# Kernel optimization log

Hardware: AMD Instinct MI355X
Metric: run time of the kernel (lower is better)

The kernel has to match this reference:

```python
import jax, jax.numpy as jnp
import numpy as np

N_NODES = 100000
N_EDGES = 1600000
D_FEAT = 64


def setup_inputs() -> dict:
    key = jax.random.key(0)
    k1, k2, k3 = jax.random.split(key, 3)
    h = jax.random.normal(k1, (N_NODES, D_FEAT), dtype=jnp.float32)
    src = jax.random.randint(k2, (N_EDGES,), 0, N_NODES, dtype=jnp.int32)
    dst = jax.random.randint(k3, (N_EDGES,), 0, N_NODES, dtype=jnp.int32)
    edge_index = jnp.stack([src, dst], axis=0)  # [2, E]
    return {"h": h, "edge_index": edge_index}


def reference(h, edge_index):
    # EdgePassing: message = src node features (gather along edges)
    # Max_aggregation: per-dst-node max over incoming messages (segment max)
    src, dst = edge_index[0], edge_index[1]
    msgs = h[src]  # [E, D] gathered mailbox, never densified per-node
    agg = jax.ops.segment_max(msgs, dst, num_segments=N_NODES)  # [N, D]
    # DGL leaves nodes with no incoming messages at zero; segment_max yields -inf
    return jnp.where(jnp.isneginf(agg), jnp.zeros_like(agg), agg)
```

## Files before the change

### kernel.cpp

```cpp
#include <hip/hip_runtime.h>

#define D_FEAT 64
#define NEG_INF_BITS 0xFF800000u
#define ENC_NEG_INF  0x007FFFFFu
#define NPB 128
#define BSHIFT 7
#define TILE_E 4096
#define SP_BLOCK 512
#define BM_BLOCK 512
#define MAXB 1024

__device__ __forceinline__ unsigned enc_f32(float v) {
    unsigned b = __float_as_uint(v);
    return ((int)b >= 0) ? (b ^ 0x80000000u) : ~b;
}
__device__ __forceinline__ float dec_f32(unsigned u) {
    return (u & 0x80000000u) ? __uint_as_float(u ^ 0x80000000u) : __uint_as_float(~u);
}

__global__ void zero_kernel(int* __restrict__ p, int n) {
    int i = blockIdx.x * blockDim.x + threadIdx.x;
    if (i < n) p[i] = 0;
}

__global__ void hist_kernel(const int* __restrict__ dst, int* __restrict__ hist,
                            int E, int B) {
    __shared__ int lh[MAXB];
    for (int i = threadIdx.x; i < B; i += blockDim.x) lh[i] = 0;
    __syncthreads();
    int E4 = E >> 2;
    const int4* dst4 = (const int4*)dst;
    for (int i = blockIdx.x * blockDim.x + threadIdx.x; i < E4;
         i += gridDim.x * blockDim.x) {
        int4 d = dst4[i];
        atomicAdd(&lh[d.x >> BSHIFT], 1);
        atomicAdd(&lh[d.y >> BSHIFT], 1);
        atomicAdd(&lh[d.z >> BSHIFT], 1);
        atomicAdd(&lh[d.w >> BSHIFT], 1);
    }
    if (blockIdx.x == 0) {
        for (int i = (E4 << 2) + threadIdx.x; i < E; i += blockDim.x)
            atomicAdd(&lh[dst[i] >> BSHIFT], 1);
    }
    __syncthreads();
    for (int i = threadIdx.x; i < B; i += blockDim.x) {
        int c = lh[i];
        if (c) atomicAdd(&hist[i], c);
    }
}

__global__ void scan_kernel(const int* __restrict__ hist, int* __restrict__ bucket_start,
                            int* __restrict__ cursor, int B) {
    __shared__ int lds[MAXB];
    int tid = threadIdx.x;
    int v = (tid < B) ? hist[tid] : 0;
    lds[tid] = v;
    __syncthreads();
    for (int off = 1; off < MAXB; off <<= 1) {
        int t = (tid >= off) ? lds[tid - off] : 0;
        __syncthreads();
        lds[tid] += t;
        __syncthreads();
    }
    if (tid < B) {
        int excl = lds[tid] - v;
        bucket_start[tid] = excl;
        cursor[tid] = excl;
        if (tid == B - 1) bucket_start[B] = lds[tid];
    }
}

__global__ void scatter_pass_kernel(const int* __restrict__ src, const int* __restrict__ dst,
                                    int* __restrict__ cursor, unsigned* __restrict__ packed,
                                    int E, int B) {
    __shared__ int lcount[MAXB];
    __shared__ int lbase[MAXB];
    int tid = threadIdx.x;
    int base = blockIdx.x * TILE_E;
    int nE = min(TILE_E, E - base);

    for (int i = tid; i < B; i += SP_BLOCK) lcount[i] = 0;
    __syncthreads();

    int n4 = nE >> 2;
    const int4* dst4 = (const int4*)(dst + base);
    for (int k = tid; k < n4; k += SP_BLOCK) {
        int4 d = dst4[k];
        atomicAdd(&lcount[d.x >> BSHIFT], 1);
        atomicAdd(&lcount[d.y >> BSHIFT], 1);
        atomicAdd(&lcount[d.z >> BSHIFT], 1);
        atomicAdd(&lcount[d.w >> BSHIFT], 1);
    }
    for (int i = (n4 << 2) + tid; i < nE; i += SP_BLOCK)
        atomicAdd(&lcount[dst[base + i] >> BSHIFT], 1);
    __syncthreads();

    for (int b = tid; b < B; b += SP_BLOCK) {
        int c = lcount[b];
        lbase[b] = c ? atomicAdd(&cursor[b], c) : 0;
        lcount[b] = 0;
    }
    __syncthreads();

    for (int i = tid; i < nE; i += SP_BLOCK) {
        int d = dst[base + i];
        int b = d >> BSHIFT;
        int pos = lbase[b] + atomicAdd(&lcount[b], 1);
        packed[pos] = (unsigned)src[base + i] | ((unsigned)(d & (NPB - 1)) << 17);
    }
}

__global__ void __launch_bounds__(BM_BLOCK)
bucket_max_kernel(const float* __restrict__ h,
                  const int* __restrict__ bucket_start,
                  const unsigned* __restrict__ packed,
                  float* __restrict__ out, int N) {
    __shared__ unsigned buf[NPB * D_FEAT];
    int b = blockIdx.x;
    int tid = threadIdx.x;
    int node0 = b << BSHIFT;
    int nvals = (min(NPB, N - node0)) * D_FEAT;

    for (int i = tid; i < NPB * D_FEAT; i += BM_BLOCK) buf[i] = ENC_NEG_INF;
    __syncthreads();

    int beg = bucket_start[b];
    int end = bucket_start[b + 1];
    int wid = tid >> 6;
    int lane = tid & 63;

    for (int base = beg + (wid << 6); base < end; base += BM_BLOCK) {
        int nk = min(64, end - base);
        unsigned p = (lane < nk) ? packed[base + lane] : 0u;
        int j = 0;
        for (; j + 4 <= nk; j += 4) {
            unsigned p0 = (unsigned)__shfl((int)p, j);
            unsigned p1 = (unsigned)__shfl((int)p, j + 1);
            unsigned p2 = (unsigned)__shfl((int)p, j + 2);
            unsigned p3 = (unsigned)__shfl((int)p, j + 3);
            float v0 = h[(p0 & 0x1FFFFu) * D_FEAT + lane];
            float v1 = h[(p1 & 0x1FFFFu) * D_FEAT + lane];
            float v2 = h[(p2 & 0x1FFFFu) * D_FEAT + lane];
            float v3 = h[(p3 & 0x1FFFFu) * D_FEAT + lane];
            atomicMax(&buf[(p0 >> 17) * D_FEAT + lane], enc_f32(v0));
            atomicMax(&buf[(p1 >> 17) * D_FEAT + lane], enc_f32(v1));
            atomicMax(&buf[(p2 >> 17) * D_FEAT + lane], enc_f32(v2));
            atomicMax(&buf[(p3 >> 17) * D_FEAT + lane], enc_f32(v3));
        }
        for (; j < nk; ++j) {
            unsigned pj = (unsigned)__shfl((int)p, j);
            float v = h[(pj & 0x1FFFFu) * D_FEAT + lane];
            atomicMax(&buf[(pj >> 17) * D_FEAT + lane], enc_f32(v));
        }
    }
    __syncthreads();

    for (int i = tid; i < nvals; i += BM_BLOCK) {
        unsigned u = buf[i];
        out[node0 * D_FEAT + i] = (u == ENC_NEG_INF) ? 0.0f : dec_f32(u);
    }
}

__global__ void init_out_kernel(uint4* __restrict__ out, int n4) {
    int i = blockIdx.x * blockDim.x + threadIdx.x;
    if (i < n4) {
        uint4 v;
        v.x = NEG_INF_BITS; v.y = NEG_INF_BITS; v.z = NEG_INF_BITS; v.w = NEG_INF_BITS;
        out[i] = v;
    }
}
__global__ void scatter_max_kernel(const float* __restrict__ h, const int* __restrict__ src,
                                   const int* __restrict__ dst, float* __restrict__ out, int E) {
    int gid = blockIdx.x * blockDim.x + threadIdx.x;
    int e = gid >> 6;
    if (e >= E) return;
    int lane = gid & 63;
    float v = h[src[e] * D_FEAT + lane];
    int* addr = (int*)(out + dst[e] * D_FEAT + lane);
    if (v >= 0.0f) atomicMax(addr, __float_as_int(v));
    else           atomicMin((unsigned int*)addr, __float_as_uint(v));
}
__global__ void finalize_kernel(float* __restrict__ out, int n) {
    int i = blockIdx.x * blockDim.x + threadIdx.x;
    if (i < n && __float_as_uint(out[i]) == NEG_INF_BITS) out[i] = 0.0f;
}

extern "C" void kernel_launch(void* const* d_in, const int* in_sizes, int n_in,
                              void* d_out, int out_size, void* d_ws, size_t ws_size,
                              hipStream_t stream) {
    const float* h = (const float*)d_in[0];
    const int* edge_index = (const int*)d_in[1];
    int E = in_sizes[1] / 2;
    const int* src = edge_index;
    const int* dst = edge_index + E;
    float* out = (float*)d_out;
    int N = out_size / D_FEAT;

    int B = (N + NPB - 1) >> BSHIFT;
    size_t ws_needed = (size_t)(3 * B + 2 + E) * sizeof(int);

    if (N <= (1 << 17) && B <= MAXB && ws_size >= ws_needed) {
        int* hist         = (int*)d_ws;
        int* bucket_start = hist + B;
        int* cursor       = bucket_start + B + 1;
        unsigned* packed  = (unsigned*)(cursor + B);

        zero_kernel<<<(B + 255) / 256, 256, 0, stream>>>(hist, B);
        hist_kernel<<<512, 256, 0, stream>>>(dst, hist, E, B);
        scan_kernel<<<1, MAXB, 0, stream>>>(hist, bucket_start, cursor, B);
        int ntiles = (E + TILE_E - 1) / TILE_E;
        scatter_pass_kernel<<<ntiles, SP_BLOCK, 0, stream>>>(src, dst, cursor, packed, E, B);
        bucket_max_kernel<<<B, BM_BLOCK, 0, stream>>>(h, bucket_start, packed, out, N);
    } else {
        int n4 = out_size / 4;
        init_out_kernel<<<(n4 + 255) / 256, 256, 0, stream>>>((uint4*)out, n4);
        long long total = (long long)E * 64;
        scatter_max_kernel<<<(int)((total + 255) / 256), 256, 0, stream>>>(h, src, dst, out, E);
        finalize_kernel<<<(out_size + 255) / 256, 256, 0, stream>>>(out, out_size);
    }
}
```

Before: 178.1 us.

## Replace global-atomic bucket sort with per-tile counts and column scan

The bucketing pipeline now stores per-tile bucket counts in workspace, computes per-tile offsets with a column-wise wave scan, and places edges using those precomputed offsets. This removes the global zero kernel, the global histogram atomics and the per-tile global cursor atomics, and it avoids counting dst twice. Tiles become much larger (T=256 blocks), so placement has less parallelism and uses more workspace. The bucket_max gather loop is also unrolled from 4 to 8 so more loads are in flight.

After: 163.5 us. 1.09x faster.

```diff
diff --git a/kernel.cpp b/kernel.cpp
--- a/kernel.cpp
+++ b/kernel.cpp
@@ -5,8 +5,6 @@
 #define ENC_NEG_INF  0x007FFFFFu
 #define NPB 128
 #define BSHIFT 7
-#define TILE_E 4096
-#define SP_BLOCK 512
 #define BM_BLOCK 512
 #define MAXB 1024
 
@@ -18,39 +16,55 @@
     return (u & 0x80000000u) ? __uint_as_float(u ^ 0x80000000u) : __uint_as_float(~u);
 }
 
-__global__ void zero_kernel(int* __restrict__ p, int n) {
-    int i = blockIdx.x * blockDim.x + threadIdx.x;
-    if (i < n) p[i] = 0;
-}
-
-__global__ void hist_kernel(const int* __restrict__ dst, int* __restrict__ hist,
-                            int E, int B) {
+__global__ void count_kernel(const int* __restrict__ dst, int* __restrict__ counts,
+                             int E, int Te, int B) {
     __shared__ int lh[MAXB];
     for (int i = threadIdx.x; i < B; i += blockDim.x) lh[i] = 0;
     __syncthreads();
-    int E4 = E >> 2;
-    const int4* dst4 = (const int4*)dst;
-    for (int i = blockIdx.x * blockDim.x + threadIdx.x; i < E4;
-         i += gridDim.x * blockDim.x) {
-        int4 d = dst4[i];
+    int t = blockIdx.x;
+    int beg = t * Te;
+    int end = min(E, beg + Te);
+    int nE = (end > beg) ? (end - beg) : 0;
+    int n4 = nE >> 2;
+    const int4* d4 = (const int4*)(dst + beg);
+    for (int k = threadIdx.x; k < n4; k += blockDim.x) {
+        int4 d = d4[k];
         atomicAdd(&lh[d.x >> BSHIFT], 1);
         atomicAdd(&lh[d.y >> BSHIFT], 1);
         atomicAdd(&lh[d.z >> BSHIFT], 1);
         atomicAdd(&lh[d.w >> BSHIFT], 1);
     }
-    if (blockIdx.x == 0) {
-        for (int i = (E4 << 2) + threadIdx.x; i < E; i += blockDim.x)
-            atomicAdd(&lh[dst[i] >> BSHIFT], 1);
-    }
-    __syncthreads();
-    for (int i = threadIdx.x; i < B; i += blockDim.x) {
-        int c = lh[i];
-        if (c) atomicAdd(&hist[i], c);
-    }
+    for (int i = beg + (n4 << 2) + threadIdx.x; i < end; i += blockDim.x)
+        atomicAdd(&lh[dst[i] >> BSHIFT], 1);
+    __syncthreads();
+    for (int i = threadIdx.x; i < B; i += blockDim.x) counts[t * B + i] = lh[i];
+}
+
+__global__ void colscan_kernel(int* __restrict__ counts, int* __restrict__ hist,
+                               int T, int B) {
+    int w = (blockIdx.x * blockDim.x + threadIdx.x) >> 6;
+    int lane = threadIdx.x & 63;
+    if (w >= B) return;
+    int b = w;
+    int R = T >> 6;
+    int v[4], pre[4];
+    int base_t = lane * R;
+    for (int r = 0; r < R; ++r) v[r] = counts[(base_t + r) * B + b];
+    int s = 0;
+    for (int r = 0; r < R; ++r) { pre[r] = s; s += v[r]; }
+    int incl = s;
+    for (int off = 1; off < 64; off <<= 1) {
+        int tup = __shfl_up(incl, off);
+        if (lane >= off) incl += tup;
+    }
+    int excl = incl - s;
+    for (int r = 0; r < R; ++r) counts[(base_t + r) * B + b] = excl + pre[r];
+    int total = __shfl(incl, 63);
+    if (lane == 0) hist[b] = total;
 }
 
 __global__ void scan_kernel(const int* __restrict__ hist, int* __restrict__ bucket_start,
-                            int* __restrict__ cursor, int B) {
+                            int B) {
     __shared__ int lds[MAXB];
     int tid = threadIdx.x;
     int v = (tid < B) ? hist[tid] : 0;
@@ -63,50 +77,26 @@
         __syncthreads();
     }
     if (tid < B) {
-        int excl = lds[tid] - v;
-        bucket_start[tid] = excl;
-        cursor[tid] = excl;
+        bucket_start[tid] = lds[tid] - v;
         if (tid == B - 1) bucket_start[B] = lds[tid];
     }
 }
 
-__global__ void scatter_pass_kernel(const int* __restrict__ src, const int* __restrict__ dst,
-                                    int* __restrict__ cursor, unsigned* __restrict__ packed,
-                                    int E, int B) {
-    __shared__ int lcount[MAXB];
-    __shared__ int lbase[MAXB];
-    int tid = threadIdx.x;
-    int base = blockIdx.x * TILE_E;
-    int nE = min(TILE_E, E - base);
-
-    for (int i = tid; i < B; i += SP_BLOCK) lcount[i] = 0;
-    __syncthreads();
-
-    int n4 = nE >> 2;
-    const int4* dst4 = (const int4*)(dst + base);
-    for (int k = tid; k < n4; k += SP_BLOCK) {
-        int4 d = dst4[k];
-        atomicAdd(&lcount[d.x >> BSHIFT], 1);
-        atomicAdd(&lcount[d.y >> BSHIFT], 1);
-        atomicAdd(&lcount[d.z >> BSHIFT], 1);
-        atomicAdd(&lcount[d.w >> BSHIFT], 1);
-    }
-    for (int i = (n4 << 2) + tid; i < nE; i += SP_BLOCK)
-        atomicAdd(&lcount[dst[base + i] >> BSHIFT], 1);
-    __syncthreads();
-
-    for (int b = tid; b < B; b += SP_BLOCK) {
-        int c = lcount[b];
-        lbase[b] = c ? atomicAdd(&cursor[b], c) : 0;
-        lcount[b] = 0;
-    }
-    __syncthreads();
-
-    for (int i = tid; i < nE; i += SP_BLOCK) {
-        int d = dst[base + i];
+__global__ void place_kernel(const int* __restrict__ src, const int* __restrict__ dst,
+                             const int* __restrict__ counts, const int* __restrict__ bucket_start,
+                             unsigned* __restrict__ packed, int E, int Te, int B) {
+    __shared__ int lcur[MAXB];
+    int t = blockIdx.x;
+    for (int i = threadIdx.x; i < B; i += blockDim.x)
+        lcur[i] = bucket_start[i] + counts[t * B + i];
+    __syncthreads();
+    int beg = t * Te;
+    int end = min(E, beg + Te);
+    for (int i = beg + threadIdx.x; i < end; i += blockDim.x) {
+        int d = dst[i];
         int b = d >> BSHIFT;
-        int pos = lbase[b] + atomicAdd(&lcount[b], 1);
-        packed[pos] = (unsigned)src[base + i] | ((unsigned)(d & (NPB - 1)) << 17);
+        int pos = atomicAdd(&lcur[b], 1);
+        packed[pos] = (unsigned)src[i] | ((unsigned)(d & (NPB - 1)) << 17);
     }
 }
 
@@ -133,19 +123,16 @@
         int nk = min(64, end - base);
         unsigned p = (lane < nk) ? packed[base + lane] : 0u;
         int j = 0;
-        for (; j + 4 <= nk; j += 4) {
-            unsigned p0 = (unsigned)__shfl((int)p, j);
-            unsigned p1 = (unsigned)__shfl((int)p, j + 1);
-            unsigned p2 = (unsigned)__shfl((int)p, j + 2);
-            unsigned p3 = (unsigned)__shfl((int)p, j + 3);
-            float v0 = h[(p0 & 0x1FFFFu) * D_FEAT + lane];
-            float v1 = h[(p1 & 0x1FFFFu) * D_FEAT + lane];
-            float v2 = h[(p2 & 0x1FFFFu) * D_FEAT + lane];
-            float v3 = h[(p3 & 0x1FFFFu) * D_FEAT + lane];
-            atomicMax(&buf[(p0 >> 17) * D_FEAT + lane], enc_f32(v0));
-            atomicMax(&buf[(p1 >> 17) * D_FEAT + lane], enc_f32(v1));
-            atomicMax(&buf[(p2 >> 17) * D_FEAT + lane], enc_f32(v2));
-            atomicMax(&buf[(p3 >> 17) * D_FEAT + lane], enc_f32(v3));
+        for (; j + 8 <= nk; j += 8) {
+            unsigned q[8];
+            float v[8];
+            #pragma unroll
+            for (int k = 0; k < 8; ++k) q[k] = (unsigned)__shfl((int)p, j + k);
+            #pragma unroll
+            for (int k = 0; k < 8; ++k) v[k] = h[(q[k] & 0x1FFFFu) * D_FEAT + lane];
+            #pragma unroll
+            for (int k = 0; k < 8; ++k)
+                atomicMax(&buf[(q[k] >> 17) * D_FEAT + lane], enc_f32(v[k]));
         }
         for (; j < nk; ++j) {
             unsigned pj = (unsigned)__shfl((int)p, j);
@@ -197,19 +184,26 @@
     int N = out_size / D_FEAT;
 
     int B = (N + NPB - 1) >> BSHIFT;
-    size_t ws_needed = (size_t)(3 * B + 2 + E) * sizeof(int);
-
-    if (N <= (1 << 17) && B <= MAXB && ws_size >= ws_needed) {
-        int* hist         = (int*)d_ws;
+
+    int T = 0;
+    for (int cand = 256; cand >= 64; cand >>= 1) {
+        size_t need = ((size_t)cand * B + B + (B + 1) + (size_t)E) * sizeof(int);
+        if (ws_size >= need) { T = cand; break; }
+    }
+
+    if (N <= (1 << 17) && B <= MAXB && T > 0) {
+        int* counts       = (int*)d_ws;
+        int* hist         = counts + (size_t)T * B;
         int* bucket_start = hist + B;
-        int* cursor       = bucket_start + B + 1;
-        unsigned* packed  = (unsigned*)(cursor + B);
-
-        zero_kernel<<<(B + 255) / 256, 256, 0, stream>>>(hist, B);
-        hist_kernel<<<512, 256, 0, stream>>>(dst, hist, E, B);
-        scan_kernel<<<1, MAXB, 0, stream>>>(hist, bucket_start, cursor, B);
-        int ntiles = (E + TILE_E - 1) / TILE_E;
-        scatter_pass_kernel<<<ntiles, SP_BLOCK, 0, stream>>>(src, dst, cursor, packed, E, B);
+        unsigned* packed  = (unsigned*)(bucket_start + B + 1);
+
+        int Te = ((E + T - 1) / T + 3) & ~3;
+
+        count_kernel<<<T, 512, 0, stream>>>(dst, counts, E, Te, B);
+        int cs_blocks = (B * 64 + 511) / 512;
+        colscan_kernel<<<cs_blocks, 512, 0, stream>>>(counts, hist, T, B);
+        scan_kernel<<<1, MAXB, 0, stream>>>(hist, bucket_start, B);
+        place_kernel<<<T, 512, 0, stream>>>(src, dst, counts, bucket_start, packed, E, Te, B);
         bucket_max_kernel<<<B, BM_BLOCK, 0, stream>>>(h, bucket_start, packed, out, N);
     } else {
         int n4 = out_size / 4;
```
